# Performance work log

Measured on AMD Instinct MI355X. Metric: run time of the kernel, lower is better.

Reference implementation:

```python
import jax, jax.numpy as jnp
import numpy as np

CARDS = [1000000, 500000, 100000, 50000, 10000, 10000, 5000, 5000, 1000, 1000,
         500, 500, 100, 100, 50, 50, 20, 20, 10, 10, 5, 5, 3, 3, 2, 2]

def _emb_dim(card):
    return int(min(32, max(4, round(1.6 * card ** 0.56))))

DIMS = [_emb_dim(c) for c in CARDS]          # per-table embedding dims (torch rule)
ROWS = [c + 1 for c in CARDS]                # +1 for UNK row at index 0 (padding_idx)
OFFS = np.concatenate([[0], np.cumsum(ROWS)[:-1]]).astype(np.int64)
TOTAL_ROWS = int(sum(ROWS))
MAX_D = 32
NUM_CONT = 64
B = 131072
CAT_DIM = int(sum(DIMS))                     # 508
FUSED_IN = CAT_DIM + 32                      # cont MLP outputs 32
LN_EPS = 1e-5


def setup_inputs() -> dict:
    key = jax.random.key(0)
    ks = jax.random.split(key, 10)
    x_cont = jax.random.normal(ks[0], (B, NUM_CONT), dtype=jnp.float32)
    # per-column indices in [0, card_i] (0 = UNK/padding)
    cols = [jax.random.randint(jax.random.fold_in(ks[1], i), (B,), 0, r, dtype=jnp.int64)
            for i, r in enumerate(ROWS)]
    x_cat = jnp.stack(cols, axis=1)  # [B, 26] int64
    # all tables stacked into one flat [TOTAL_ROWS, 32] array; table i uses cols [:DIMS[i]]
    emb_flat = jax.random.normal(ks[2], (TOTAL_ROWS, MAX_D), dtype=jnp.float32) * 0.05
    emb_flat = emb_flat.at[np.asarray(OFFS)].set(0.0)  # padding_idx=0 rows are zero
    # cont MLP: Linear(64,32) + LayerNorm(32) + SiLU
    Wc = jax.random.normal(ks[3], (NUM_CONT, 32), dtype=jnp.float32) * (1.0 / np.sqrt(NUM_CONT))
    bc = jnp.zeros((32,), jnp.float32)
    ln_g = jnp.ones((32,), jnp.float32)
    ln_b = jnp.zeros((32,), jnp.float32)
    # proj: Linear(540,64)+SiLU, Linear(64,32)+SiLU (dropout = identity in eval)
    W1 = jax.random.normal(ks[4], (FUSED_IN, 64), dtype=jnp.float32) * (1.0 / np.sqrt(FUSED_IN))
    b1 = jnp.zeros((64,), jnp.float32)
    W2 = jax.random.normal(ks[5], (64, 32), dtype=jnp.float32) * (1.0 / np.sqrt(64))
    b2 = jnp.zeros((32,), jnp.float32)
    return {"x_cont": x_cont, "x_cat": x_cat, "emb_flat": emb_flat,
            "Wc": Wc, "bc": bc, "ln_g": ln_g, "ln_b": ln_b,
            "W1": W1, "b1": b1, "W2": W2, "b2": b2}


def reference(x_cont, x_cat, emb_flat, Wc, bc, ln_g, ln_b, W1, b1, W2, b2):
    # --- multi-table embedding gather + concat (eval: dropout = identity) ---
    gidx = x_cat + jnp.asarray(OFFS)[None, :]          # [B, T] global row ids
    rows = emb_flat[gidx]                               # [B, T, 32] single fused gather
    rows = rows * (x_cat != 0).astype(rows.dtype)[..., None]  # padding_idx semantics
    cat = jnp.concatenate([rows[:, i, :d] for i, d in enumerate(DIMS)], axis=1)  # [B, 508]
    # --- cont MLP: Linear + LayerNorm + SiLU ---
    h = x_cont @ Wc + bc                                # [B, 32]
    mu = jnp.mean(h, axis=-1, keepdims=True)
    var = jnp.var(h, axis=-1, keepdims=True)
    h = (h - mu) / jnp.sqrt(var + LN_EPS) * ln_g + ln_b
    h = jax.nn.silu(h)
    # --- fuse + proj MLP ---
    fused = jnp.concatenate([h, cat], axis=1)           # [B, 540]
    z = jax.nn.silu(fused @ W1 + b1)                    # [B, 64]
    z = jax.nn.silu(z @ W2 + b2)                        # [B, 32]
    return z
```

## Files before the change

### kernel.cpp

```cpp
#include <hip/hip_runtime.h>

typedef __attribute__((ext_vector_type(8))) short bf16x8;
typedef __attribute__((ext_vector_type(4))) float f32x4;

#define NT 26
#define BROWS 32
#define NKS 19
#define LDSTR 616
#define Z1STR 68
#define WS_FRAG_DWORDS 19456

__constant__ int c_OFFS[NT] = {
    0,1000001,1500002,1600003,1650004,1660005,1670006,1675007,1680008,1681009,
    1682010,1682511,1683012,1683113,1683214,1683265,1683316,1683337,1683358,
    1683369,1683380,1683386,1683392,1683396,1683400,1683403};

__constant__ int c_P_COLP[NT] = {
    0,32,64,96,128,160,192,224,256,288,320,352,384,416,448,464,480,496,
    512,520,528,532,536,540,544,548};
__constant__ int c_P_DIMS[NT] = {
    32,32,32,32,32,32,32,32,32,32,32,32,21,21,14,14,9,9,6,6,4,4,4,4,4,4};
__constant__ int c_P_COLF[NT] = {
    0,32,64,96,128,160,192,224,256,288,320,352,384,405,426,440,454,463,
    472,478,484,488,492,496,500,504};

__device__ __forceinline__ unsigned short f2bf(float f) {
  unsigned int u = __builtin_bit_cast(unsigned int, f);
  u += 0x7fffu + ((u >> 16) & 1u);
  return (unsigned short)(u >> 16);
}

__device__ __forceinline__ unsigned cvtpk(float a, float b) {
  unsigned r;
  asm("v_cvt_pk_bf16_f32 %0, %1, %2" : "=v"(r) : "v"(a), "v"(b));
  return r;
}

__device__ __forceinline__ uint2 pk2(float4 a) {
  uint2 o;
  o.x = cvtpk(a.x, a.y); o.y = cvtpk(a.z, a.w);
  return o;
}

__device__ __forceinline__ float silu_f(float x) {
  return x / (1.0f + __expf(-x));
}

extern "C" __global__ void __launch_bounds__(256)
prep_w1(const float* __restrict__ W1, unsigned int* __restrict__ wsf) {
  const int g = blockIdx.x * 256 + threadIdx.x;
  if (g >= WS_FRAG_DWORDS) return;
  const int f  = g * 2;
  const int j  = f & 7;
  const int l  = (f >> 3) & 63;
  const int w  = (f >> 9) & 3;
  const int ks = f >> 11;
  const int bn = (w << 4) + (l & 15);
  const int k0 = (ks << 5) + ((l >> 4) << 3) + j;
  float v[2];
  #pragma unroll
  for (int e = 0; e < 2; ++e) {
    const int k = k0 + e;
    float x = 0.0f;
    if (k < 32) {
      x = W1[k * 64 + bn];
    } else {
      const int c = k - 32;
      for (int i = 0; i < NT; ++i) {
        const int off = c - c_P_COLP[i];
        if (off >= 0 && off < c_P_DIMS[i])
          x = W1[(32 + c_P_COLF[i] + off) * 64 + bn];
      }
    }
    v[e] = x;
  }
  wsf[g] = ((unsigned)f2bf(v[0])) | (((unsigned)f2bf(v[1])) << 16);
}

extern "C" __global__ void __launch_bounds__(256, 2)
tab_fused(const float* __restrict__ xc,
          const int* __restrict__ xcat,
          const float* __restrict__ emb,
          const float* __restrict__ Wc,
          const float* __restrict__ bc,
          const float* __restrict__ lng,
          const float* __restrict__ lnb,
          const unsigned short* __restrict__ wsf,
          const float* __restrict__ b1,
          const float* __restrict__ W2,
          const float* __restrict__ b2,
          float* __restrict__ out) {
  __shared__ __attribute__((aligned(16))) float smem[(BROWS * LDSTR) / 2];
  __shared__ __attribute__((aligned(16))) int xs[BROWS * NT];
  unsigned short* fused = (unsigned short*)smem;
  char* tbb = (char*)smem;
  float* z1 = smem;

  const int t  = threadIdx.x;
  const int w  = t >> 6;
  const int l  = t & 63;
  const int R0 = blockIdx.x * BROWS;

  const int bn = (w << 4) + (l & 15);
  const int kg = (l >> 4) << 3;

  if (t < 208) ((int4*)xs)[t] = ((const int4*)(xcat + (size_t)R0 * NT))[t];
  if (t >= 160) {
    const int tt = t - 160;
    uint4 zz = {0u, 0u, 0u, 0u};
    *(uint4*)(tbb + (tt / 3) * (LDSTR * 2) + 1168 + (tt % 3) * 16) = zz;
  }
  __syncthreads();

  const int rowA = (w << 3) + (l >> 3);
  const int qA = l & 7;
  float4 vA[14];
  #pragma unroll
  for (int u = 0; u < 14; ++u) {
    const int idx = xs[rowA * NT + u];
    vA[u] = *(const float4*)(emb + ((size_t)(c_OFFS[u] + idx) << 5) + (qA << 2));
  }
  const int pbb = (w << 4) + (l >> 2);
  const int rowB = pbb & 31;
  const int qB = l & 3;
  float4 vB[2];
  #pragma unroll
  for (int u = 0; u < 2; ++u) {
    const int tab = 14 + (u << 1) + (pbb >> 5);
    const int idx = xs[rowB * NT + tab];
    vB[u] = *(const float4*)(emb + ((size_t)(c_OFFS[tab] + idx) << 5) + (qB << 2));
  }
  const bool hasC = (w < 2);
  const int rowC = l >> 1, qC = l & 1, tabC = 18 + w;
  float4 vC = {0.f, 0.f, 0.f, 0.f};
  if (hasC) {
    const int idx = xs[rowC * NT + tabC];
    vC = *(const float4*)(emb + ((size_t)(c_OFFS[tabC] + idx) << 5) + (qC << 2));
  }
  const bool hasD = (w != 1);
  const int dD = (w == 2) ? 0 : ((w == 3) ? 1 : 2);
  const int tabD = 20 + (dD << 1) + (l >> 5);
  const int rowD = l & 31;
  float4 vD = {0.f, 0.f, 0.f, 0.f};
  if (hasD) {
    const int idx = xs[rowD * NT + tabD];
    vD = *(const float4*)(emb + ((size_t)(c_OFFS[tabD] + idx) << 5));
  }

  {
    const int r  = t >> 3;
    const int j0 = (t & 7) << 2;
    const float* xr = xc + (size_t)(R0 + r) * 64;
    float h0 = bc[j0], h1 = bc[j0 + 1], h2 = bc[j0 + 2], h3 = bc[j0 + 3];
    #pragma unroll 4
    for (int k4 = 0; k4 < 16; ++k4) {
      const float4 x4 = ((const float4*)xr)[k4];
      const float* wb = Wc + (k4 * 4) * 32 + j0;
      const float4 w0 = *(const float4*)(wb);
      const float4 w1 = *(const float4*)(wb + 32);
      const float4 w2 = *(const float4*)(wb + 64);
      const float4 w3 = *(const float4*)(wb + 96);
      h0 = __fmaf_rn(x4.x, w0.x, h0); h1 = __fmaf_rn(x4.x, w0.y, h1);
      h2 = __fmaf_rn(x4.x, w0.z, h2); h3 = __fmaf_rn(x4.x, w0.w, h3);
      h0 = __fmaf_rn(x4.y, w1.x, h0); h1 = __fmaf_rn(x4.y, w1.y, h1);
      h2 = __fmaf_rn(x4.y, w1.z, h2); h3 = __fmaf_rn(x4.y, w1.w, h3);
      h0 = __fmaf_rn(x4.z, w2.x, h0); h1 = __fmaf_rn(x4.z, w2.y, h1);
      h2 = __fmaf_rn(x4.z, w2.z, h2); h3 = __fmaf_rn(x4.z, w2.w, h3);
      h0 = __fmaf_rn(x4.w, w3.x, h0); h1 = __fmaf_rn(x4.w, w3.y, h1);
      h2 = __fmaf_rn(x4.w, w3.z, h2); h3 = __fmaf_rn(x4.w, w3.w, h3);
    }
    float s1v = h0 + h1 + h2 + h3;
    float s2v = h0 * h0 + h1 * h1 + h2 * h2 + h3 * h3;
    #pragma unroll
    for (int m = 1; m < 8; m <<= 1) {
      s1v += __shfl_xor(s1v, m);
      s2v += __shfl_xor(s2v, m);
    }
    const float mu = s1v * 0.03125f;
    const float var = s2v * 0.03125f - mu * mu;
    const float rs = rsqrtf(var + 1e-5f);
    const float g0 = silu_f((h0 - mu) * rs * lng[j0]     + lnb[j0]);
    const float g1 = silu_f((h1 - mu) * rs * lng[j0 + 1] + lnb[j0 + 1]);
    const float g2 = silu_f((h2 - mu) * rs * lng[j0 + 2] + lnb[j0 + 2]);
    const float g3 = silu_f((h3 - mu) * rs * lng[j0 + 3] + lnb[j0 + 3]);
    uint2 hw;
    hw.x = cvtpk(g0, g1);
    hw.y = cvtpk(g2, g3);
    *(uint2*)(tbb + r * (LDSTR * 2) + j0 * 2) = hw;
  }

  {
    char* dA = tbb + rowA * (LDSTR * 2) + 64 + qA * 8;
    #pragma unroll
    for (int u = 0; u < 14; ++u) *(uint2*)(dA + u * 64) = pk2(vA[u]);
    char* dB = tbb + rowB * (LDSTR * 2) + 960 + (pbb >> 5) * 32 + qB * 8;
    #pragma unroll
    for (int u = 0; u < 2; ++u) *(uint2*)(dB + u * 64) = pk2(vB[u]);
    if (hasC)
      *(uint2*)(tbb + rowC * (LDSTR * 2) + 1088 + w * 16 + qC * 8) = pk2(vC);
    if (hasD)
      *(uint2*)(tbb + rowD * (LDSTR * 2) + 1120 +
                (((dD << 1) + (l >> 5)) << 3)) = pk2(vD);
  }

  bf16x8 bfw[NKS];
  #pragma unroll
  for (int ks = 0; ks < NKS; ++ks)
    bfw[ks] = *(const bf16x8*)(wsf + ((ks * 4 + w) * 64 + l) * 8);
  __syncthreads();

  f32x4 acc[2];
  acc[0] = (f32x4){0.f, 0.f, 0.f, 0.f};
  acc[1] = (f32x4){0.f, 0.f, 0.f, 0.f};
  const unsigned short* arow0 = &fused[(l & 15) * LDSTR + kg];
  const unsigned short* arow1 = arow0 + 16 * LDSTR;
  #pragma unroll
  for (int ks = 0; ks < NKS; ++ks) {
    acc[0] = __builtin_amdgcn_mfma_f32_16x16x32_bf16(
        *(const bf16x8*)(arow0 + (ks << 5)), bfw[ks], acc[0], 0, 0, 0);
    acc[1] = __builtin_amdgcn_mfma_f32_16x16x32_bf16(
        *(const bf16x8*)(arow1 + (ks << 5)), bfw[ks], acc[1], 0, 0, 0);
  }
  __syncthreads();

  {
    const float b1v = b1[bn];
    const int rb = (l >> 4) << 2;
    #pragma unroll
    for (int mt = 0; mt < 2; ++mt) {
      #pragma unroll
      for (int v = 0; v < 4; ++v) {
        const int row = (mt << 4) + rb + v;
        z1[row * Z1STR + bn] = silu_f(acc[mt][v] + b1v);
      }
    }
  }
  __syncthreads();

  {
    const int r  = t >> 3;
    const int j0 = (t & 7) << 2;
    float a0 = b2[j0], a1 = b2[j0 + 1], a2 = b2[j0 + 2], a3 = b2[j0 + 3];
    const float4* zr4 = (const float4*)&z1[r * Z1STR];
    #pragma unroll
    for (int k4 = 0; k4 < 16; ++k4) {
      const float4 zv = zr4[k4];
      const float* w2b = W2 + (k4 * 4) * 32 + j0;
      const float4 w0 = *(const float4*)(w2b);
      const float4 w1 = *(const float4*)(w2b + 32);
      const float4 w2v = *(const float4*)(w2b + 64);
      const float4 w3 = *(const float4*)(w2b + 96);
      a0 = __fmaf_rn(zv.x, w0.x, a0); a1 = __fmaf_rn(zv.x, w0.y, a1);
      a2 = __fmaf_rn(zv.x, w0.z, a2); a3 = __fmaf_rn(zv.x, w0.w, a3);
      a0 = __fmaf_rn(zv.y, w1.x, a0); a1 = __fmaf_rn(zv.y, w1.y, a1);
      a2 = __fmaf_rn(zv.y, w1.z, a2); a3 = __fmaf_rn(zv.y, w1.w, a3);
      a0 = __fmaf_rn(zv.z, w2v.x, a0); a1 = __fmaf_rn(zv.z, w2v.y, a1);
      a2 = __fmaf_rn(zv.z, w2v.z, a2); a3 = __fmaf_rn(zv.z, w2v.w, a3);
      a0 = __fmaf_rn(zv.w, w3.x, a0); a1 = __fmaf_rn(zv.w, w3.y, a1);
      a2 = __fmaf_rn(zv.w, w3.z, a2); a3 = __fmaf_rn(zv.w, w3.w, a3);
    }
    float4 o;
    o.x = silu_f(a0); o.y = silu_f(a1); o.z = silu_f(a2); o.w = silu_f(a3);
    *(float4*)(out + (size_t)(R0 + r) * 32 + j0) = o;
  }
}

extern "C" void kernel_launch(void* const* d_in, const int* in_sizes, int n_in,
                              void* d_out, int out_size, void* d_ws, size_t ws_size,
                              hipStream_t stream) {
  const float* xc   = (const float*)d_in[0];
  const int*   xcat = (const int*)  d_in[1];
  const float* emb  = (const float*)d_in[2];
  const float* Wc   = (const float*)d_in[3];
  const float* bc   = (const float*)d_in[4];
  const float* lng  = (const float*)d_in[5];
  const float* lnb  = (const float*)d_in[6];
  const float* W1   = (const float*)d_in[7];
  const float* b1   = (const float*)d_in[8];
  const float* W2   = (const float*)d_in[9];
  const float* b2   = (const float*)d_in[10];
  float* out = (float*)d_out;

  unsigned int* wsf = (unsigned int*)d_ws;
  hipLaunchKernelGGL(prep_w1, dim3((WS_FRAG_DWORDS + 255) / 256), dim3(256),
                     0, stream, W1, wsf);

  const int B = in_sizes[0] / 64;
  const int grid = B / BROWS;
  hipLaunchKernelGGL(tab_fused, dim3(grid), dim3(256), 0, stream,
                     xc, xcat, emb, Wc, bc, lng, lnb,
                     (const unsigned short*)wsf, b1, W2, b2, out);
}
```

Before: 112.8 us.

## Halve rows per block to 16 and remap gather and MLP work per thread

Cuts the batch tile from 32 to 16 rows per block. The embedding gather, the continuous MLP and the second-layer work are re-split so each thread does half as much (7 tables instead of 14, 2 outputs instead of 4). Each wave now issues a single MFMA tile per k-step. The aim is more blocks, smaller per-thread register and LDS footprint and higher occupancy to hide gather latency, at the cost of reloading the B-fragment weights once per 16 rows instead of per 32.

```diff
diff --git a/kernel.cpp b/kernel.cpp
--- a/kernel.cpp
+++ b/kernel.cpp
@@ -4,7 +4,7 @@
 typedef __attribute__((ext_vector_type(4))) float f32x4;
 
 #define NT 26
-#define BROWS 32
+#define BROWS 16
 #define NKS 19
 #define LDSTR 616
 #define Z1STR 68
@@ -104,103 +104,82 @@
   const int bn = (w << 4) + (l & 15);
   const int kg = (l >> 4) << 3;
 
-  if (t < 208) ((int4*)xs)[t] = ((const int4*)(xcat + (size_t)R0 * NT))[t];
-  if (t >= 160) {
-    const int tt = t - 160;
+  if (t < 104) ((int4*)xs)[t] = ((const int4*)(xcat + (size_t)R0 * NT))[t];
+  if (t < 48) {
     uint4 zz = {0u, 0u, 0u, 0u};
-    *(uint4*)(tbb + (tt / 3) * (LDSTR * 2) + 1168 + (tt % 3) * 16) = zz;
-  }
-  __syncthreads();
-
-  const int rowA = (w << 3) + (l >> 3);
+    *(uint4*)(tbb + (t / 3) * (LDSTR * 2) + 1168 + (t % 3) * 16) = zz;
+  }
+  __syncthreads();
+
+  const int rowA = ((w & 1) << 3) + (l >> 3);
   const int qA = l & 7;
-  float4 vA[14];
-  #pragma unroll
-  for (int u = 0; u < 14; ++u) {
-    const int idx = xs[rowA * NT + u];
-    vA[u] = *(const float4*)(emb + ((size_t)(c_OFFS[u] + idx) << 5) + (qA << 2));
-  }
-  const int pbb = (w << 4) + (l >> 2);
-  const int rowB = pbb & 31;
-  const int qB = l & 3;
-  float4 vB[2];
-  #pragma unroll
-  for (int u = 0; u < 2; ++u) {
-    const int tab = 14 + (u << 1) + (pbb >> 5);
-    const int idx = xs[rowB * NT + tab];
-    vB[u] = *(const float4*)(emb + ((size_t)(c_OFFS[tab] + idx) << 5) + (qB << 2));
-  }
-  const bool hasC = (w < 2);
-  const int rowC = l >> 1, qC = l & 1, tabC = 18 + w;
+  const int u0 = (w >> 1) * 7;
+  float4 vA[7];
+  #pragma unroll
+  for (int u = 0; u < 7; ++u) {
+    const int idx = xs[rowA * NT + u0 + u];
+    vA[u] = *(const float4*)(emb + ((size_t)(c_OFFS[u0 + u] + idx) << 5) + (qA << 2));
+  }
+  const int rB = t >> 4;
+  const int tB = (t >> 2) & 3;
+  const int qB = t & 3;
+  const int idxB = xs[rB * NT + 14 + tB];
+  const float4 vB = *(const float4*)(emb + ((size_t)(c_OFFS[14 + tB] + idxB) << 5) + (qB << 2));
+  const bool hasC = (t < 64);
+  const int rowC = t >> 2, tabC = 18 + ((t >> 1) & 1), qC = t & 1;
   float4 vC = {0.f, 0.f, 0.f, 0.f};
   if (hasC) {
-    const int idx = xs[rowC * NT + tabC];
-    vC = *(const float4*)(emb + ((size_t)(c_OFFS[tabC] + idx) << 5) + (qC << 2));
-  }
-  const bool hasD = (w != 1);
-  const int dD = (w == 2) ? 0 : ((w == 3) ? 1 : 2);
-  const int tabD = 20 + (dD << 1) + (l >> 5);
-  const int rowD = l & 31;
+    const int idxC = xs[rowC * NT + tabC];
+    vC = *(const float4*)(emb + ((size_t)(c_OFFS[tabC] + idxC) << 5) + (qC << 2));
+  }
+  const int rowD = t >> 3, slotD = t & 7;
+  const bool hasD = (t < 128) && (slotD < 6);
   float4 vD = {0.f, 0.f, 0.f, 0.f};
   if (hasD) {
-    const int idx = xs[rowD * NT + tabD];
-    vD = *(const float4*)(emb + ((size_t)(c_OFFS[tabD] + idx) << 5));
-  }
-
-  {
-    const int r  = t >> 3;
-    const int j0 = (t & 7) << 2;
-    const float* xr = xc + (size_t)(R0 + r) * 64;
-    float h0 = bc[j0], h1 = bc[j0 + 1], h2 = bc[j0 + 2], h3 = bc[j0 + 3];
+    const int idxD = xs[rowD * NT + 20 + slotD];
+    vD = *(const float4*)(emb + ((size_t)(c_OFFS[20 + slotD] + idxD) << 5));
+  }
+
+  {
+    const int rH = t >> 4;
+    const int jH = (t & 15) << 1;
+    const float* xr = xc + (size_t)(R0 + rH) * 64;
+    float h0 = bc[jH], h1 = bc[jH + 1];
     #pragma unroll 4
     for (int k4 = 0; k4 < 16; ++k4) {
       const float4 x4 = ((const float4*)xr)[k4];
-      const float* wb = Wc + (k4 * 4) * 32 + j0;
-      const float4 w0 = *(const float4*)(wb);
-      const float4 w1 = *(const float4*)(wb + 32);
-      const float4 w2 = *(const float4*)(wb + 64);
-      const float4 w3 = *(const float4*)(wb + 96);
-      h0 = __fmaf_rn(x4.x, w0.x, h0); h1 = __fmaf_rn(x4.x, w0.y, h1);
-      h2 = __fmaf_rn(x4.x, w0.z, h2); h3 = __fmaf_rn(x4.x, w0.w, h3);
-      h0 = __fmaf_rn(x4.y, w1.x, h0); h1 = __fmaf_rn(x4.y, w1.y, h1);
-      h2 = __fmaf_rn(x4.y, w1.z, h2); h3 = __fmaf_rn(x4.y, w1.w, h3);
-      h0 = __fmaf_rn(x4.z, w2.x, h0); h1 = __fmaf_rn(x4.z, w2.y, h1);
-      h2 = __fmaf_rn(x4.z, w2.z, h2); h3 = __fmaf_rn(x4.z, w2.w, h3);
-      h0 = __fmaf_rn(x4.w, w3.x, h0); h1 = __fmaf_rn(x4.w, w3.y, h1);
-      h2 = __fmaf_rn(x4.w, w3.z, h2); h3 = __fmaf_rn(x4.w, w3.w, h3);
-    }
-    float s1v = h0 + h1 + h2 + h3;
-    float s2v = h0 * h0 + h1 * h1 + h2 * h2 + h3 * h3;
+      #pragma unroll
+      for (int kk = 0; kk < 4; ++kk) {
+        const float xk = (kk == 0) ? x4.x : (kk == 1) ? x4.y : (kk == 2) ? x4.z : x4.w;
+        const float2 wv = *(const float2*)(Wc + (k4 * 4 + kk) * 32 + jH);
+        h0 = __fmaf_rn(xk, wv.x, h0);
+        h1 = __fmaf_rn(xk, wv.y, h1);
+      }
+    }
+    float s1 = h0 + h1;
+    float s2 = h0 * h0 + h1 * h1;
     #pragma unroll
-    for (int m = 1; m < 8; m <<= 1) {
-      s1v += __shfl_xor(s1v, m);
-      s2v += __shfl_xor(s2v, m);
-    }
-    const float mu = s1v * 0.03125f;
-    const float var = s2v * 0.03125f - mu * mu;
+    for (int m = 1; m < 16; m <<= 1) {
+      s1 += __shfl_xor(s1, m);
+      s2 += __shfl_xor(s2, m);
+    }
+    const float mu = s1 * 0.03125f;
+    const float var = s2 * 0.03125f - mu * mu;
     const float rs = rsqrtf(var + 1e-5f);
-    const float g0 = silu_f((h0 - mu) * rs * lng[j0]     + lnb[j0]);
-    const float g1 = silu_f((h1 - mu) * rs * lng[j0 + 1] + lnb[j0 + 1]);
-    const float g2 = silu_f((h2 - mu) * rs * lng[j0 + 2] + lnb[j0 + 2]);
-    const float g3 = silu_f((h3 - mu) * rs * lng[j0 + 3] + lnb[j0 + 3]);
-    uint2 hw;
-    hw.x = cvtpk(g0, g1);
-    hw.y = cvtpk(g2, g3);
-    *(uint2*)(tbb + r * (LDSTR * 2) + j0 * 2) = hw;
-  }
-
-  {
-    char* dA = tbb + rowA * (LDSTR * 2) + 64 + qA * 8;
+    const float g0 = silu_f((h0 - mu) * rs * lng[jH]     + lnb[jH]);
+    const float g1 = silu_f((h1 - mu) * rs * lng[jH + 1] + lnb[jH + 1]);
+    *(unsigned*)(tbb + rH * (LDSTR * 2) + jH * 2) = cvtpk(g0, g1);
+  }
+
+  {
+    char* dA = tbb + rowA * (LDSTR * 2) + 64 + u0 * 64 + qA * 8;
     #pragma unroll
-    for (int u = 0; u < 14; ++u) *(uint2*)(dA + u * 64) = pk2(vA[u]);
-    char* dB = tbb + rowB * (LDSTR * 2) + 960 + (pbb >> 5) * 32 + qB * 8;
-    #pragma unroll
-    for (int u = 0; u < 2; ++u) *(uint2*)(dB + u * 64) = pk2(vB[u]);
+    for (int u = 0; u < 7; ++u) *(uint2*)(dA + u * 64) = pk2(vA[u]);
+    *(uint2*)(tbb + rB * (LDSTR * 2) + 960 + tB * 32 + qB * 8) = pk2(vB);
     if (hasC)
-      *(uint2*)(tbb + rowC * (LDSTR * 2) + 1088 + w * 16 + qC * 8) = pk2(vC);
+      *(uint2*)(tbb + rowC * (LDSTR * 2) + 1088 + (tabC - 18) * 16 + qC * 8) = pk2(vC);
     if (hasD)
-      *(uint2*)(tbb + rowD * (LDSTR * 2) + 1120 +
-                (((dD << 1) + (l >> 5)) << 3)) = pk2(vD);
+      *(uint2*)(tbb + rowD * (LDSTR * 2) + 1120 + slotD * 8) = pk2(vD);
   }
 
   bf16x8 bfw[NKS];
@@ -209,59 +188,44 @@
     bfw[ks] = *(const bf16x8*)(wsf + ((ks * 4 + w) * 64 + l) * 8);
   __syncthreads();
 
-  f32x4 acc[2];
-  acc[0] = (f32x4){0.f, 0.f, 0.f, 0.f};
-  acc[1] = (f32x4){0.f, 0.f, 0.f, 0.f};
+  f32x4 acc = (f32x4){0.f, 0.f, 0.f, 0.f};
   const unsigned short* arow0 = &fused[(l & 15) * LDSTR + kg];
-  const unsigned short* arow1 = arow0 + 16 * LDSTR;
   #pragma unroll
   for (int ks = 0; ks < NKS; ++ks) {
-    acc[0] = __builtin_amdgcn_mfma_f32_16x16x32_bf16(
-        *(const bf16x8*)(arow0 + (ks << 5)), bfw[ks], acc[0], 0, 0, 0);
-    acc[1] = __builtin_amdgcn_mfma_f32_16x16x32_bf16(
-        *(const bf16x8*)(arow1 + (ks << 5)), bfw[ks], acc[1], 0, 0, 0);
+    acc = __builtin_amdgcn_mfma_f32_16x16x32_bf16(
+        *(const bf16x8*)(arow0 + (ks << 5)), bfw[ks], acc, 0, 0, 0);
   }
   __syncthreads();
 
   {
     const float b1v = b1[bn];
-    const int rb = (l >> 4) << 2;
+    const int rb2 = (l >> 4) << 2;
     #pragma unroll
-    for (int mt = 0; mt < 2; ++mt) {
-      #pragma unroll
-      for (int v = 0; v < 4; ++v) {
-        const int row = (mt << 4) + rb + v;
-        z1[row * Z1STR + bn] = silu_f(acc[mt][v] + b1v);
-      }
-    }
-  }
-  __syncthreads();
-
-  {
-    const int r  = t >> 3;
-    const int j0 = (t & 7) << 2;
-    float a0 = b2[j0], a1 = b2[j0 + 1], a2 = b2[j0 + 2], a3 = b2[j0 + 3];
+    for (int v = 0; v < 4; ++v)
+      z1[(rb2 + v) * Z1STR + bn] = silu_f(acc[v] + b1v);
+  }
+  __syncthreads();
+
+  {
+    const int r  = t >> 4;
+    const int j0 = (t & 15) << 1;
+    float a0 = b2[j0], a1 = b2[j0 + 1];
     const float4* zr4 = (const float4*)&z1[r * Z1STR];
-    #pragma unroll
+    #pragma unroll 4
     for (int k4 = 0; k4 < 16; ++k4) {
       const float4 zv = zr4[k4];
-      const float* w2b = W2 + (k4 * 4) * 32 + j0;
-      const float4 w0 = *(const float4*)(w2b);
-      const float4 w1 = *(const float4*)(w2b + 32);
-      const float4 w2v = *(const float4*)(w2b + 64);
-      const float4 w3 = *(const float4*)(w2b + 96);
-      a0 = __fmaf_rn(zv.x, w0.x, a0); a1 = __fmaf_rn(zv.x, w0.y, a1);
-      a2 = __fmaf_rn(zv.x, w0.z, a2); a3 = __fmaf_rn(zv.x, w0.w, a3);
-      a0 = __fmaf_rn(zv.y, w1.x, a0); a1 = __fmaf_rn(zv.y, w1.y, a1);
-      a2 = __fmaf_rn(zv.y, w1.z, a2); a3 = __fmaf_rn(zv.y, w1.w, a3);
-      a0 = __fmaf_rn(zv.z, w2v.x, a0); a1 = __fmaf_rn(zv.z, w2v.y, a1);
-      a2 = __fmaf_rn(zv.z, w2v.z, a2); a3 = __fmaf_rn(zv.z, w2v.w, a3);
-      a0 = __fmaf_rn(zv.w, w3.x, a0); a1 = __fmaf_rn(zv.w, w3.y, a1);
-      a2 = __fmaf_rn(zv.w, w3.z, a2); a3 = __fmaf_rn(zv.w, w3.w, a3);
-    }
-    float4 o;
-    o.x = silu_f(a0); o.y = silu_f(a1); o.z = silu_f(a2); o.w = silu_f(a3);
-    *(float4*)(out + (size_t)(R0 + r) * 32 + j0) = o;
+      #pragma unroll
+      for (int kk = 0; kk < 4; ++kk) {
+        const float zk = (kk == 0) ? zv.x : (kk == 1) ? zv.y : (kk == 2) ? zv.z : zv.w;
+        const float2 wv = *(const float2*)(W2 + (k4 * 4 + kk) * 32 + j0);
+        a0 = __fmaf_rn(zk, wv.x, a0);
+        a1 = __fmaf_rn(zk, wv.y, a1);
+      }
+    }
+    float2 o;
+    o.x = silu_f(a0);
+    o.y = silu_f(a1);
+    *(float2*)(out + (size_t)(R0 + r) * 32 + j0) = o;
   }
 }
 
```

New measurement: 178.1 us. 1.58x slower.

## Make blocks persistent over four row tiles with software-pipelined embedding gathers

Applied to the files above, without the earlier changes.

Each block now processes four 32-row tiles in a loop and prefetches the next tile's categorical indices and embedding rows into registers while running the MFMA for the current tile. The grid shrinks by four, which amortises block launch and setup. The W1 fragments are now streamed from global memory through a four-deep rolling buffer instead of holding all 19 in registers, which lowers register pressure but re-reads them for every tile. Risks are fewer blocks to hide latency across CUs and an extra barrier per tile.

```diff
diff --git a/kernel.cpp b/kernel.cpp
--- a/kernel.cpp
+++ b/kernel.cpp
@@ -5,6 +5,7 @@
 
 #define NT 26
 #define BROWS 32
+#define TILES 4
 #define NKS 19
 #define LDSTR 616
 #define Z1STR 68
@@ -77,6 +78,29 @@
   wsf[g] = ((unsigned)f2bf(v[0])) | (((unsigned)f2bf(v[1])) << 16);
 }
 
+#define GATHER_ISSUE()                                                        \
+  {                                                                           \
+    _Pragma("unroll")                                                         \
+    for (int u = 0; u < 14; ++u) {                                            \
+      const int idx = xs[rowA * NT + u];                                      \
+      vA[u] = *(const float4*)(emb + ((size_t)(c_OFFS[u] + idx) << 5) + (qA << 2)); \
+    }                                                                         \
+    _Pragma("unroll")                                                         \
+    for (int u = 0; u < 2; ++u) {                                             \
+      const int tab = 14 + (u << 1) + (pbb >> 5);                             \
+      const int idx = xs[rowB * NT + tab];                                    \
+      vB[u] = *(const float4*)(emb + ((size_t)(c_OFFS[tab] + idx) << 5) + (qB << 2)); \
+    }                                                                         \
+    if (hasC) {                                                               \
+      const int idx = xs[rowC * NT + tabC];                                   \
+      vC = *(const float4*)(emb + ((size_t)(c_OFFS[tabC] + idx) << 5) + (qC << 2)); \
+    }                                                                         \
+    if (hasD) {                                                               \
+      const int idx = xs[rowD * NT + tabD];                                   \
+      vD = *(const float4*)(emb + ((size_t)(c_OFFS[tabD] + idx) << 5));       \
+    }                                                                         \
+  }
+
 extern "C" __global__ void __launch_bounds__(256, 2)
 tab_fused(const float* __restrict__ xc,
           const int* __restrict__ xcat,
@@ -99,169 +123,166 @@
   const int t  = threadIdx.x;
   const int w  = t >> 6;
   const int l  = t & 63;
-  const int R0 = blockIdx.x * BROWS;
+  const int T0 = blockIdx.x * TILES;
 
   const int bn = (w << 4) + (l & 15);
   const int kg = (l >> 4) << 3;
 
-  if (t < 208) ((int4*)xs)[t] = ((const int4*)(xcat + (size_t)R0 * NT))[t];
-  if (t >= 160) {
-    const int tt = t - 160;
-    uint4 zz = {0u, 0u, 0u, 0u};
-    *(uint4*)(tbb + (tt / 3) * (LDSTR * 2) + 1168 + (tt % 3) * 16) = zz;
+  const int rowA = (w << 3) + (l >> 3), qA = l & 7;
+  const int pbb = (w << 4) + (l >> 2), rowB = pbb & 31, qB = l & 3;
+  const bool hasC = (w < 2);
+  const int rowC = l >> 1, tabC = 18 + w, qC = l & 1;
+  const bool hasD = (w != 1);
+  const int dD = (w == 2) ? 0 : ((w == 3) ? 1 : 2);
+  const int tabD = 20 + (dD << 1) + (l >> 5), rowD = l & 31;
+  const int rH = t >> 3, jH = (t & 7) << 2;
+  const float b1v = b1[bn];
+
+  const unsigned short* arow0 = &fused[(l & 15) * LDSTR + kg];
+  const unsigned short* arow1 = arow0 + 16 * LDSTR;
+
+  float4 vA[14], vB[2];
+  float4 vC = {0.f, 0.f, 0.f, 0.f}, vD = {0.f, 0.f, 0.f, 0.f};
+  int4 xv = {0, 0, 0, 0};
+  if (t < 208) {
+    xv = ((const int4*)(xcat + (size_t)(T0 * BROWS) * NT))[t];
+    ((int4*)xs)[t] = xv;
   }
   __syncthreads();
-
-  const int rowA = (w << 3) + (l >> 3);
-  const int qA = l & 7;
-  float4 vA[14];
-  #pragma unroll
-  for (int u = 0; u < 14; ++u) {
-    const int idx = xs[rowA * NT + u];
-    vA[u] = *(const float4*)(emb + ((size_t)(c_OFFS[u] + idx) << 5) + (qA << 2));
-  }
-  const int pbb = (w << 4) + (l >> 2);
-  const int rowB = pbb & 31;
-  const int qB = l & 3;
-  float4 vB[2];
-  #pragma unroll
-  for (int u = 0; u < 2; ++u) {
-    const int tab = 14 + (u << 1) + (pbb >> 5);
-    const int idx = xs[rowB * NT + tab];
-    vB[u] = *(const float4*)(emb + ((size_t)(c_OFFS[tab] + idx) << 5) + (qB << 2));
-  }
-  const bool hasC = (w < 2);
-  const int rowC = l >> 1, qC = l & 1, tabC = 18 + w;
-  float4 vC = {0.f, 0.f, 0.f, 0.f};
-  if (hasC) {
-    const int idx = xs[rowC * NT + tabC];
-    vC = *(const float4*)(emb + ((size_t)(c_OFFS[tabC] + idx) << 5) + (qC << 2));
-  }
-  const bool hasD = (w != 1);
-  const int dD = (w == 2) ? 0 : ((w == 3) ? 1 : 2);
-  const int tabD = 20 + (dD << 1) + (l >> 5);
-  const int rowD = l & 31;
-  float4 vD = {0.f, 0.f, 0.f, 0.f};
-  if (hasD) {
-    const int idx = xs[rowD * NT + tabD];
-    vD = *(const float4*)(emb + ((size_t)(c_OFFS[tabD] + idx) << 5));
-  }
-
-  {
-    const int r  = t >> 3;
-    const int j0 = (t & 7) << 2;
-    const float* xr = xc + (size_t)(R0 + r) * 64;
-    float h0 = bc[j0], h1 = bc[j0 + 1], h2 = bc[j0 + 2], h3 = bc[j0 + 3];
-    #pragma unroll 4
-    for (int k4 = 0; k4 < 16; ++k4) {
-      const float4 x4 = ((const float4*)xr)[k4];
-      const float* wb = Wc + (k4 * 4) * 32 + j0;
-      const float4 w0 = *(const float4*)(wb);
-      const float4 w1 = *(const float4*)(wb + 32);
-      const float4 w2 = *(const float4*)(wb + 64);
-      const float4 w3 = *(const float4*)(wb + 96);
-      h0 = __fmaf_rn(x4.x, w0.x, h0); h1 = __fmaf_rn(x4.x, w0.y, h1);
-      h2 = __fmaf_rn(x4.x, w0.z, h2); h3 = __fmaf_rn(x4.x, w0.w, h3);
-      h0 = __fmaf_rn(x4.y, w1.x, h0); h1 = __fmaf_rn(x4.y, w1.y, h1);
-      h2 = __fmaf_rn(x4.y, w1.z, h2); h3 = __fmaf_rn(x4.y, w1.w, h3);
-      h0 = __fmaf_rn(x4.z, w2.x, h0); h1 = __fmaf_rn(x4.z, w2.y, h1);
-      h2 = __fmaf_rn(x4.z, w2.z, h2); h3 = __fmaf_rn(x4.z, w2.w, h3);
-      h0 = __fmaf_rn(x4.w, w3.x, h0); h1 = __fmaf_rn(x4.w, w3.y, h1);
-      h2 = __fmaf_rn(x4.w, w3.z, h2); h3 = __fmaf_rn(x4.w, w3.w, h3);
-    }
-    float s1v = h0 + h1 + h2 + h3;
-    float s2v = h0 * h0 + h1 * h1 + h2 * h2 + h3 * h3;
-    #pragma unroll
-    for (int m = 1; m < 8; m <<= 1) {
-      s1v += __shfl_xor(s1v, m);
-      s2v += __shfl_xor(s2v, m);
-    }
-    const float mu = s1v * 0.03125f;
-    const float var = s2v * 0.03125f - mu * mu;
-    const float rs = rsqrtf(var + 1e-5f);
-    const float g0 = silu_f((h0 - mu) * rs * lng[j0]     + lnb[j0]);
-    const float g1 = silu_f((h1 - mu) * rs * lng[j0 + 1] + lnb[j0 + 1]);
-    const float g2 = silu_f((h2 - mu) * rs * lng[j0 + 2] + lnb[j0 + 2]);
-    const float g3 = silu_f((h3 - mu) * rs * lng[j0 + 3] + lnb[j0 + 3]);
+  GATHER_ISSUE();
+  if (t < 208)
+    xv = ((const int4*)(xcat + (size_t)((T0 + 1) * BROWS) * NT))[t];
+  __builtin_amdgcn_sched_barrier(0);
+  __syncthreads();
+
+  #pragma unroll 1
+  for (int n = 0; n < TILES; ++n) {
+    const int R0 = (T0 + n) * BROWS;
+
     uint2 hw;
-    hw.x = cvtpk(g0, g1);
-    hw.y = cvtpk(g2, g3);
-    *(uint2*)(tbb + r * (LDSTR * 2) + j0 * 2) = hw;
-  }
-
-  {
-    char* dA = tbb + rowA * (LDSTR * 2) + 64 + qA * 8;
-    #pragma unroll
-    for (int u = 0; u < 14; ++u) *(uint2*)(dA + u * 64) = pk2(vA[u]);
-    char* dB = tbb + rowB * (LDSTR * 2) + 960 + (pbb >> 5) * 32 + qB * 8;
-    #pragma unroll
-    for (int u = 0; u < 2; ++u) *(uint2*)(dB + u * 64) = pk2(vB[u]);
-    if (hasC)
-      *(uint2*)(tbb + rowC * (LDSTR * 2) + 1088 + w * 16 + qC * 8) = pk2(vC);
-    if (hasD)
-      *(uint2*)(tbb + rowD * (LDSTR * 2) + 1120 +
-                (((dD << 1) + (l >> 5)) << 3)) = pk2(vD);
-  }
-
-  bf16x8 bfw[NKS];
-  #pragma unroll
-  for (int ks = 0; ks < NKS; ++ks)
-    bfw[ks] = *(const bf16x8*)(wsf + ((ks * 4 + w) * 64 + l) * 8);
-  __syncthreads();
-
-  f32x4 acc[2];
-  acc[0] = (f32x4){0.f, 0.f, 0.f, 0.f};
-  acc[1] = (f32x4){0.f, 0.f, 0.f, 0.f};
-  const unsigned short* arow0 = &fused[(l & 15) * LDSTR + kg];
-  const unsigned short* arow1 = arow0 + 16 * LDSTR;
-  #pragma unroll
-  for (int ks = 0; ks < NKS; ++ks) {
-    acc[0] = __builtin_amdgcn_mfma_f32_16x16x32_bf16(
-        *(const bf16x8*)(arow0 + (ks << 5)), bfw[ks], acc[0], 0, 0, 0);
-    acc[1] = __builtin_amdgcn_mfma_f32_16x16x32_bf16(
-        *(const bf16x8*)(arow1 + (ks << 5)), bfw[ks], acc[1], 0, 0, 0);
-  }
-  __syncthreads();
-
-  {
-    const float b1v = b1[bn];
-    const int rb = (l >> 4) << 2;
-    #pragma unroll
-    for (int mt = 0; mt < 2; ++mt) {
-      #pragma unroll
-      for (int v = 0; v < 4; ++v) {
-        const int row = (mt << 4) + rb + v;
-        z1[row * Z1STR + bn] = silu_f(acc[mt][v] + b1v);
-      }
-    }
-  }
-  __syncthreads();
-
-  {
-    const int r  = t >> 3;
-    const int j0 = (t & 7) << 2;
-    float a0 = b2[j0], a1 = b2[j0 + 1], a2 = b2[j0 + 2], a3 = b2[j0 + 3];
-    const float4* zr4 = (const float4*)&z1[r * Z1STR];
-    #pragma unroll
-    for (int k4 = 0; k4 < 16; ++k4) {
-      const float4 zv = zr4[k4];
-      const float* w2b = W2 + (k4 * 4) * 32 + j0;
-      const float4 w0 = *(const float4*)(w2b);
-      const float4 w1 = *(const float4*)(w2b + 32);
-      const float4 w2v = *(const float4*)(w2b + 64);
-      const float4 w3 = *(const float4*)(w2b + 96);
-      a0 = __fmaf_rn(zv.x, w0.x, a0); a1 = __fmaf_rn(zv.x, w0.y, a1);
-      a2 = __fmaf_rn(zv.x, w0.z, a2); a3 = __fmaf_rn(zv.x, w0.w, a3);
-      a0 = __fmaf_rn(zv.y, w1.x, a0); a1 = __fmaf_rn(zv.y, w1.y, a1);
-      a2 = __fmaf_rn(zv.y, w1.z, a2); a3 = __fmaf_rn(zv.y, w1.w, a3);
-      a0 = __fmaf_rn(zv.z, w2v.x, a0); a1 = __fmaf_rn(zv.z, w2v.y, a1);
-      a2 = __fmaf_rn(zv.z, w2v.z, a2); a3 = __fmaf_rn(zv.z, w2v.w, a3);
-      a0 = __fmaf_rn(zv.w, w3.x, a0); a1 = __fmaf_rn(zv.w, w3.y, a1);
-      a2 = __fmaf_rn(zv.w, w3.z, a2); a3 = __fmaf_rn(zv.w, w3.w, a3);
-    }
-    float4 o;
-    o.x = silu_f(a0); o.y = silu_f(a1); o.z = silu_f(a2); o.w = silu_f(a3);
-    *(float4*)(out + (size_t)(R0 + r) * 32 + j0) = o;
+    {
+      const float* xr = xc + (size_t)(R0 + rH) * 64;
+      float h0 = bc[jH], h1 = bc[jH + 1], h2 = bc[jH + 2], h3 = bc[jH + 3];
+      #pragma unroll 4
+      for (int k4 = 0; k4 < 16; ++k4) {
+        const float4 x4 = ((const float4*)xr)[k4];
+        const float* wb = Wc + (k4 * 4) * 32 + jH;
+        const float4 w0 = *(const float4*)(wb);
+        const float4 w1 = *(const float4*)(wb + 32);
+        const float4 w2 = *(const float4*)(wb + 64);
+        const float4 w3 = *(const float4*)(wb + 96);
+        h0 = __fmaf_rn(x4.x, w0.x, h0); h1 = __fmaf_rn(x4.x, w0.y, h1);
+        h2 = __fmaf_rn(x4.x, w0.z, h2); h3 = __fmaf_rn(x4.x, w0.w, h3);
+        h0 = __fmaf_rn(x4.y, w1.x, h0); h1 = __fmaf_rn(x4.y, w1.y, h1);
+        h2 = __fmaf_rn(x4.y, w1.z, h2); h3 = __fmaf_rn(x4.y, w1.w, h3);
+        h0 = __fmaf_rn(x4.z, w2.x, h0); h1 = __fmaf_rn(x4.z, w2.y, h1);
+        h2 = __fmaf_rn(x4.z, w2.z, h2); h3 = __fmaf_rn(x4.z, w2.w, h3);
+        h0 = __fmaf_rn(x4.w, w3.x, h0); h1 = __fmaf_rn(x4.w, w3.y, h1);
+        h2 = __fmaf_rn(x4.w, w3.z, h2); h3 = __fmaf_rn(x4.w, w3.w, h3);
+      }
+      float s1v = h0 + h1 + h2 + h3;
+      float s2v = h0 * h0 + h1 * h1 + h2 * h2 + h3 * h3;
+      #pragma unroll
+      for (int m = 1; m < 8; m <<= 1) {
+        s1v += __shfl_xor(s1v, m);
+        s2v += __shfl_xor(s2v, m);
+      }
+      const float mu = s1v * 0.03125f;
+      const float var = s2v * 0.03125f - mu * mu;
+      const float rs = rsqrtf(var + 1e-5f);
+      const float g0 = silu_f((h0 - mu) * rs * lng[jH]     + lnb[jH]);
+      const float g1 = silu_f((h1 - mu) * rs * lng[jH + 1] + lnb[jH + 1]);
+      const float g2 = silu_f((h2 - mu) * rs * lng[jH + 2] + lnb[jH + 2]);
+      const float g3 = silu_f((h3 - mu) * rs * lng[jH + 3] + lnb[jH + 3]);
+      hw.x = cvtpk(g0, g1);
+      hw.y = cvtpk(g2, g3);
+    }
+
+    *(uint2*)(tbb + rH * (LDSTR * 2) + jH * 2) = hw;
+    {
+      char* dA = tbb + rowA * (LDSTR * 2) + 64 + qA * 8;
+      #pragma unroll
+      for (int u = 0; u < 14; ++u) *(uint2*)(dA + u * 64) = pk2(vA[u]);
+      char* dB = tbb + rowB * (LDSTR * 2) + 960 + (pbb >> 5) * 32 + qB * 8;
+      #pragma unroll
+      for (int u = 0; u < 2; ++u) *(uint2*)(dB + u * 64) = pk2(vB[u]);
+      if (hasC)
+        *(uint2*)(tbb + rowC * (LDSTR * 2) + 1088 + w * 16 + qC * 8) = pk2(vC);
+      if (hasD)
+        *(uint2*)(tbb + rowD * (LDSTR * 2) + 1120 +
+                  (((dD << 1) + (l >> 5)) << 3)) = pk2(vD);
+    }
+    if (t >= 160) {
+      const int tt = t - 160;
+      uint4 zz = {0u, 0u, 0u, 0u};
+      *(uint4*)(tbb + (tt / 3) * (LDSTR * 2) + 1168 + (tt % 3) * 16) = zz;
+    }
+    if (n + 1 < TILES && t < 208) ((int4*)xs)[t] = xv;
+    __syncthreads();
+
+    if (n + 1 < TILES) {
+      GATHER_ISSUE();
+      if (n + 2 < TILES && t < 208)
+        xv = ((const int4*)(xcat + (size_t)((T0 + n + 2) * BROWS) * NT))[t];
+      __builtin_amdgcn_sched_barrier(0);
+    }
+
+    f32x4 acc0 = {0.f, 0.f, 0.f, 0.f};
+    f32x4 acc1 = {0.f, 0.f, 0.f, 0.f};
+    {
+      bf16x8 bwbuf[4];
+      #pragma unroll
+      for (int p = 0; p < 4; ++p)
+        bwbuf[p] = *(const bf16x8*)(wsf + ((p * 4 + w) * 64 + l) * 8);
+      #pragma unroll
+      for (int ks = 0; ks < NKS; ++ks) {
+        const bf16x8 bw = bwbuf[ks & 3];
+        if (ks + 4 < NKS)
+          bwbuf[ks & 3] = *(const bf16x8*)(wsf + (((ks + 4) * 4 + w) * 64 + l) * 8);
+        acc0 = __builtin_amdgcn_mfma_f32_16x16x32_bf16(
+            *(const bf16x8*)(arow0 + (ks << 5)), bw, acc0, 0, 0, 0);
+        acc1 = __builtin_amdgcn_mfma_f32_16x16x32_bf16(
+            *(const bf16x8*)(arow1 + (ks << 5)), bw, acc1, 0, 0, 0);
+      }
+    }
+    __syncthreads();
+
+    {
+      const int rb = (l >> 4) << 2;
+      #pragma unroll
+      for (int v = 0; v < 4; ++v)
+        z1[(rb + v) * Z1STR + bn] = silu_f(acc0[v] + b1v);
+      #pragma unroll
+      for (int v = 0; v < 4; ++v)
+        z1[(16 + rb + v) * Z1STR + bn] = silu_f(acc1[v] + b1v);
+    }
+    __syncthreads();
+
+    {
+      float a0 = b2[jH], a1 = b2[jH + 1], a2 = b2[jH + 2], a3 = b2[jH + 3];
+      const float4* zr4 = (const float4*)&z1[rH * Z1STR];
+      #pragma unroll
+      for (int k4 = 0; k4 < 16; ++k4) {
+        const float4 zv = zr4[k4];
+        const float* w2b = W2 + (k4 * 4) * 32 + jH;
+        const float4 w0 = *(const float4*)(w2b);
+        const float4 w1 = *(const float4*)(w2b + 32);
+        const float4 w2v = *(const float4*)(w2b + 64);
+        const float4 w3 = *(const float4*)(w2b + 96);
+        a0 = __fmaf_rn(zv.x, w0.x, a0); a1 = __fmaf_rn(zv.x, w0.y, a1);
+        a2 = __fmaf_rn(zv.x, w0.z, a2); a3 = __fmaf_rn(zv.x, w0.w, a3);
+        a0 = __fmaf_rn(zv.y, w1.x, a0); a1 = __fmaf_rn(zv.y, w1.y, a1);
+        a2 = __fmaf_rn(zv.y, w1.z, a2); a3 = __fmaf_rn(zv.y, w1.w, a3);
+        a0 = __fmaf_rn(zv.z, w2v.x, a0); a1 = __fmaf_rn(zv.z, w2v.y, a1);
+        a2 = __fmaf_rn(zv.z, w2v.z, a2); a3 = __fmaf_rn(zv.z, w2v.w, a3);
+        a0 = __fmaf_rn(zv.w, w3.x, a0); a1 = __fmaf_rn(zv.w, w3.y, a1);
+        a2 = __fmaf_rn(zv.w, w3.z, a2); a3 = __fmaf_rn(zv.w, w3.w, a3);
+      }
+      float4 o;
+      o.x = silu_f(a0); o.y = silu_f(a1); o.z = silu_f(a2); o.w = silu_f(a3);
+      *(float4*)(out + (size_t)(R0 + rH) * 32 + jH) = o;
+    }
+    __syncthreads();
   }
 }
 
@@ -286,7 +307,7 @@
                      0, stream, W1, wsf);
 
   const int B = in_sizes[0] / 64;
-  const int grid = B / BROWS;
+  const int grid = B / (BROWS * TILES);
   hipLaunchKernelGGL(tab_fused, dim3(grid), dim3(256), 0, stream,
                      xc, xcat, emb, Wc, bc, lng, lnb,
                      (const unsigned short*)wsf, b1, W2, b2, out);
```

Measured after the change: 165.9 us. 47.1% more time.
